# Kernel optimization log

Measured on AMD Instinct MI355X. Metric: run time of the kernel, lower is better.

Reference implementation:

```python
import jax, jax.numpy as jnp
import numpy as np

B, H, L, D = 4, 16, 2048, 128


def setup_inputs() -> dict:
    key = jax.random.key(0)
    kx, kw1, kb1, kw2, kb2 = jax.random.split(key, 5)
    s = 1.0 / np.sqrt(D)
    return {
        "x": jax.random.normal(kx, (B, H, L, D), dtype=jnp.float32),
        "W1": jax.random.uniform(kw1, (D, D), jnp.float32, -s, s),
        "b1": jax.random.uniform(kb1, (D,), jnp.float32, -s, s),
        "W2": jax.random.uniform(kw2, (D, D), jnp.float32, -s, s),
        "b2": jax.random.uniform(kb2, (D,), jnp.float32, -s, s),
    }


def reference(x, W1, b1, W2, b2):
    # proj_1/proj_2: Linear(dim, dim) on the last axis (torch stores W as [out,in])
    q = jnp.einsum('bhld,ed->bhle', x, W1) + b1  # [B,H,L,D]
    k = jnp.einsum('bhld,ed->bhle', x, W2) + b2  # [B,H,L,D]
    # exact-erf GELU on raw QK^T scores, then softmax over j
    adj = jax.nn.gelu(jnp.einsum('bhid,bhjd->bhij', q, k), approximate=False)
    adj = jax.nn.softmax(adj, axis=-1)  # [B,H,L,L]
    # dropout is identity in eval mode
    out = jnp.einsum('bhij,bhjd->bhid', adj, x)  # [B,H,L,D]
    return out.transpose(0, 2, 1, 3).reshape(B, L, H * D)
```

## Files before the change

### kernel.cpp

```cpp
#include <hip/hip_runtime.h>
#include <hip/hip_bf16.h>

#define B_ 4
#define H_ 16
#define L_ 2048
#define D_ 128
#define BH_ 64

typedef __attribute__((ext_vector_type(8))) _Float16 f16x8;
typedef __attribute__((ext_vector_type(4))) float f32x4;
typedef __attribute__((ext_vector_type(16))) float f32x16;
typedef __attribute__((ext_vector_type(2))) unsigned u32x2;

#define L2E 1.44269504088896f

__device__ __forceinline__ float gelu_m(float v, float negm) {
  float x    = v * 0.70710678118f;
  float ax   = __builtin_fabsf(x);
  float t    = __builtin_amdgcn_rcpf(__builtin_fmaf(0.3275911f, ax, 1.0f));
  float poly = t * __builtin_fmaf(t,
                 __builtin_fmaf(t,
                   __builtin_fmaf(t,
                     __builtin_fmaf(t, 1.061405429f, -1.453152027f),
                   1.421413741f),
                 -0.284496736f),
               0.254829592f);
  float nv   = -0.72134752f * v;
  float e    = __builtin_amdgcn_exp2f(nv * v);
  float hva  = __builtin_fabsf(nv);
  float relm = fmaxf(__builtin_fmaf(1.44269504f, v, negm), negm);
  float pe   = poly * e;
  return __builtin_fmaf(hva, -pe, relm);
}

__device__ __forceinline__ void gl2lds16(const void* g, void* l) {
  __builtin_amdgcn_global_load_lds(
      (const __attribute__((address_space(1))) void*)g,
      (__attribute__((address_space(3))) void*)l, 16, 0, 0);
}

__device__ __forceinline__ unsigned pkrtz(float a, float b) {
  auto t = __builtin_amdgcn_cvt_pkrtz(a, b);
  return __builtin_bit_cast(unsigned, t);
}

__global__ __launch_bounds__(256) void wcvt_kernel(
    const float* __restrict__ W1, const float* __restrict__ W2,
    _Float16* __restrict__ Wh1, _Float16* __restrict__ Wh2)
{
  int i = blockIdx.x * 256 + threadIdx.x;
  Wh1[i] = (_Float16)W1[i];
  Wh2[i] = (_Float16)W2[i];
}

__global__ __launch_bounds__(256) void proj_tr_kernel(
    const float* __restrict__ x,
    const _Float16* __restrict__ Wh1, const float* __restrict__ b1,
    const _Float16* __restrict__ Wh2, const float* __restrict__ b2,
    _Float16* __restrict__ Qb, _Float16* __restrict__ Kb,
    _Float16* __restrict__ VT)
{
  const int tid  = threadIdx.x;
  const int wave = tid >> 6;
  const int lane = tid & 63;
  const int lhi  = lane >> 4;
  const int llo  = lane & 15;
  const int r0   = blockIdx.x * 64;
  const int wr0  = r0 + wave * 16;

  f16x8 a[4];
#pragma unroll
  for (int ks = 0; ks < 4; ++ks) {
    const float* p = x + (size_t)(wr0 + llo) * D_ + lhi * 8 + ks * 32;
    f16x8 t;
#pragma unroll
    for (int e = 0; e < 8; ++e) t[e] = (_Float16)p[e];
    a[ks] = t;
  }

  f32x4 accq[8], acck[8];
#pragma unroll
  for (int n = 0; n < 8; ++n) {
    accq[n] = (f32x4){0.f, 0.f, 0.f, 0.f};
    acck[n] = (f32x4){0.f, 0.f, 0.f, 0.f};
  }

#pragma unroll
  for (int n = 0; n < 8; ++n) {
    const int e = n * 16 + llo;
#pragma unroll
    for (int ks = 0; ks < 4; ++ks) {
      f16x8 w1f = *(const f16x8*)(Wh1 + (size_t)e * D_ + lhi * 8 + ks * 32);
      f16x8 w2f = *(const f16x8*)(Wh2 + (size_t)e * D_ + lhi * 8 + ks * 32);
      accq[n] = __builtin_amdgcn_mfma_f32_16x16x32_f16(a[ks], w1f, accq[n], 0, 0, 0);
      acck[n] = __builtin_amdgcn_mfma_f32_16x16x32_f16(a[ks], w2f, acck[n], 0, 0, 0);
    }
  }

#pragma unroll
  for (int n = 0; n < 8; ++n) {
    const int e = n * 16 + llo;
    const float bias1 = b1[e];
    const float bias2 = b2[e];
#pragma unroll
    for (int r = 0; r < 4; ++r) {
      const size_t row = (size_t)wr0 + lhi * 4 + r;
      Qb[row * D_ + e] = (_Float16)(accq[n][r] + bias1);
      Kb[row * D_ + e] = (_Float16)(acck[n][r] + bias2);
    }
  }

  const int bh = r0 / L_;
  const int l0 = r0 % L_;
  const int d  = tid & 127;
  const int rh = tid >> 7;
  _Float16* dst = VT + (size_t)bh * D_ * L_ + (size_t)d * L_ + l0 + rh * 32;
#pragma unroll
  for (int j = 0; j < 4; ++j) {
    f16x8 t;
#pragma unroll
    for (int e = 0; e < 8; ++e)
      t[e] = (_Float16)x[(size_t)(r0 + rh * 32 + j * 8 + e) * D_ + d];
    *(f16x8*)(dst + j * 8) = t;
  }
}

__global__ __launch_bounds__(512) void attn_kernel(
    const _Float16* __restrict__ Qb, const _Float16* __restrict__ Kb,
    const _Float16* __restrict__ VT, float* __restrict__ out)
{
  __shared__ _Float16 Ks[2][64 * 128];
  __shared__ _Float16 Vs[2][128 * 64];

  const int tid  = threadIdx.x;
  const int wave = tid >> 6;
  const int lane = tid & 63;
  const int l5   = lane & 31;
  const int hi   = lane >> 5;

  const int bid = blockIdx.x;
  const int blk = (bid & 7) * 64 + (bid >> 3);
  const int bh  = blk >> 3;
  const int q0  = (blk & 7) * 256;
  const int b   = bh >> 4;
  const int h   = bh & 15;
  const int wq0 = q0 + wave * 32;

  const char* KheadB = (const char*)(Kb + (size_t)bh * L_ * D_);
  const char* VheadB = (const char*)(VT + (size_t)bh * D_ * L_);

  int klds[2], ksrc[2], vlds[2], vsrc[2];
#pragma unroll
  for (int c = 0; c < 2; ++c) {
    const int wc = wave * 2 + c;
    klds[c] = wc * 1024;
    {
      const int l  = wc * 4 + (lane >> 4);
      const int c0 = (lane & 15) * 8;
      ksrc[c] = l * 256 + 2 * (c0 ^ ((l & 7) << 3));
    }
    vlds[c] = wc * 1024;
    {
      const int d  = wc * 8 + (lane >> 3);
      const int c0 = (lane & 7) * 8;
      vsrc[c] = d * 4096 + 2 * (c0 ^ ((d & 7) << 3));
    }
  }
  const int kvswz = (l5 & 7) << 3;

  f16x8 qf[8];
#pragma unroll
  for (int s = 0; s < 8; ++s)
    qf[s] = *(const f16x8*)(Qb + ((size_t)bh * L_ + wq0 + l5) * D_ + s * 16 + hi * 8);

  f32x16 accO[4];
#pragma unroll
  for (int n = 0; n < 4; ++n)
#pragma unroll
    for (int r = 0; r < 16; ++r) accO[n][r] = 0.f;
  float negm = 64.f;
  float l = 0.f;

#pragma unroll
  for (int c = 0; c < 2; ++c) {
    gl2lds16(KheadB + ksrc[c], (char*)&Ks[0][0] + klds[c]);
    gl2lds16(VheadB + vsrc[c], (char*)&Vs[0][0] + vlds[c]);
  }
  __syncthreads();

  int cur = 0;
  for (int t = 0; t < L_ / 64; ++t) {
    if (t + 1 < L_ / 64) {
      const char* kt_ = KheadB + (size_t)(t + 1) * 64 * 256;
      const char* vt_ = VheadB + (size_t)(t + 1) * 128;
#pragma unroll
      for (int c = 0; c < 2; ++c) {
        gl2lds16(kt_ + ksrc[c], (char*)&Ks[cur ^ 1][0] + klds[c]);
        gl2lds16(vt_ + vsrc[c], (char*)&Vs[cur ^ 1][0] + vlds[c]);
      }
    }
    const _Float16* Kcur = &Ks[cur][0];
    const _Float16* Vcur = &Vs[cur][0];

#pragma unroll
    for (int kb = 0; kb < 2; ++kb) {
      f32x16 sT;
#pragma unroll
      for (int r = 0; r < 16; ++r) sT[r] = 0.f;
      __builtin_amdgcn_s_setprio(1);
#pragma unroll
      for (int s = 0; s < 8; ++s) {
        f16x8 kf = *(const f16x8*)(Kcur + (kb * 32 + l5) * 128 +
                                   ((s * 16 + hi * 8) ^ kvswz));
        sT = __builtin_amdgcn_mfma_f32_32x32x16_f16(kf, qf[s], sT, 0, 0, 0);
      }
      __builtin_amdgcn_s_setprio(0);

      float gm[16];
#pragma unroll
      for (int r = 0; r < 16; ++r) gm[r] = gelu_m(sT[r], negm);

      float tm = fmaxf(fmaxf(gm[0], gm[1]), gm[2]);
      tm = fmaxf(fmaxf(tm, gm[3]),  gm[4]);
      tm = fmaxf(fmaxf(tm, gm[5]),  gm[6]);
      tm = fmaxf(fmaxf(tm, gm[7]),  gm[8]);
      tm = fmaxf(fmaxf(tm, gm[9]),  gm[10]);
      tm = fmaxf(fmaxf(tm, gm[11]), gm[12]);
      tm = fmaxf(fmaxf(tm, gm[13]), gm[14]);
      tm = fmaxf(tm, gm[15]);
      tm = fmaxf(tm, __shfl_xor(tm, 32));

      float p[16];
      float ts;
      if (__all(tm <= 11.5415603f)) {
#pragma unroll
        for (int r = 0; r < 16; ++r) p[r] = __builtin_amdgcn_exp2f(gm[r]);
        float a0 = p[0]+p[1],   a1 = p[2]+p[3],   a2 = p[4]+p[5],   a3 = p[6]+p[7];
        float a4 = p[8]+p[9],   a5 = p[10]+p[11], a6 = p[12]+p[13], a7 = p[14]+p[15];
        ts = ((a0+a1)+(a2+a3)) + ((a4+a5)+(a6+a7));
        ts += __shfl_xor(ts, 32);
        l += ts;
      } else {
        float dm = fmaxf(tm, 0.f);
        negm -= dm;
        float sc = __builtin_amdgcn_exp2f(-dm);
#pragma unroll
        for (int r = 0; r < 16; ++r) p[r] = __builtin_amdgcn_exp2f(gm[r] - dm);
        float a0 = p[0]+p[1],   a1 = p[2]+p[3],   a2 = p[4]+p[5],   a3 = p[6]+p[7];
        float a4 = p[8]+p[9],   a5 = p[10]+p[11], a6 = p[12]+p[13], a7 = p[14]+p[15];
        ts = ((a0+a1)+(a2+a3)) + ((a4+a5)+(a6+a7));
        ts += __shfl_xor(ts, 32);
        l = __builtin_fmaf(l, sc, ts);
        float scr[16];
#pragma unroll
        for (int r = 0; r < 16; ++r)
          scr[r] = __shfl(sc, (r & 3) + 8 * (r >> 2) + 4 * hi);
#pragma unroll
        for (int n = 0; n < 4; ++n)
#pragma unroll
          for (int r = 0; r < 16; ++r) accO[n][r] *= scr[r];
      }

      unsigned pk01 = pkrtz(p[0], p[1]),   pk23 = pkrtz(p[2], p[3]);
      unsigned pk45 = pkrtz(p[4], p[5]),   pk67 = pkrtz(p[6], p[7]);
      unsigned pk89 = pkrtz(p[8], p[9]),   pkAB = pkrtz(p[10], p[11]);
      unsigned pkCD = pkrtz(p[12], p[13]), pkEF = pkrtz(p[14], p[15]);
      u32x2 r0 = __builtin_amdgcn_permlane32_swap(pk01, pk45, false, false);
      u32x2 r1 = __builtin_amdgcn_permlane32_swap(pk23, pk67, false, false);
      u32x2 r2 = __builtin_amdgcn_permlane32_swap(pk89, pkCD, false, false);
      u32x2 r3 = __builtin_amdgcn_permlane32_swap(pkAB, pkEF, false, false);
      union { unsigned u[4]; f16x8 v; } A0c, A1c;
      A0c.u[0] = r0[0]; A0c.u[1] = r1[0]; A0c.u[2] = r0[1]; A0c.u[3] = r1[1];
      A1c.u[0] = r2[0]; A1c.u[1] = r3[0]; A1c.u[2] = r2[1]; A1c.u[3] = r3[1];

      __builtin_amdgcn_s_setprio(1);
#pragma unroll
      for (int n = 0; n < 4; ++n) {
        f16x8 vf0 = *(const f16x8*)(Vcur + (n * 32 + l5) * 64 +
                                    ((kb * 32 + hi * 8) ^ kvswz));
        accO[n] = __builtin_amdgcn_mfma_f32_32x32x16_f16(A0c.v, vf0, accO[n], 0, 0, 0);
        f16x8 vf1 = *(const f16x8*)(Vcur + (n * 32 + l5) * 64 +
                                    ((kb * 32 + 16 + hi * 8) ^ kvswz));
        accO[n] = __builtin_amdgcn_mfma_f32_32x32x16_f16(A1c.v, vf1, accO[n], 0, 0, 0);
      }
      __builtin_amdgcn_s_setprio(0);
    }

    __syncthreads();
    cur ^= 1;
  }

  float linv = __builtin_amdgcn_rcpf(l);
  float lb[16];
#pragma unroll
  for (int r = 0; r < 16; ++r)
    lb[r] = __shfl(linv, (r & 3) + 8 * (r >> 2) + 4 * hi);
#pragma unroll
  for (int n = 0; n < 4; ++n)
#pragma unroll
    for (int r = 0; r < 16; ++r) {
      const int i = wq0 + (r & 3) + 8 * (r >> 2) + 4 * hi;
      out[((size_t)(b * L_ + i) * H_ + h) * D_ + n * 32 + l5] = accO[n][r] * lb[r];
    }
}

extern "C" void kernel_launch(void* const* d_in, const int* in_sizes, int n_in,
                              void* d_out, int out_size, void* d_ws, size_t ws_size,
                              hipStream_t stream) {
  const float* x  = (const float*)d_in[0];
  const float* W1 = (const float*)d_in[1];
  const float* b1 = (const float*)d_in[2];
  const float* W2 = (const float*)d_in[3];
  const float* b2 = (const float*)d_in[4];
  float* out = (float*)d_out;

  const size_t N = (size_t)BH_ * L_ * D_;
  _Float16* Qb = (_Float16*)d_ws;
  _Float16* Kb = Qb + N;
  _Float16* VT = Kb + N;

  _Float16* Wh1 = (_Float16*)d_out;
  _Float16* Wh2 = Wh1 + D_ * D_;

  wcvt_kernel<<<64, 256, 0, stream>>>(W1, W2, Wh1, Wh2);
  proj_tr_kernel<<<(BH_ * L_) / 64, 256, 0, stream>>>(x, Wh1, b1, Wh2, b2, Qb, Kb, VT);
  attn_kernel<<<BH_ * (L_ / 256), 512, 0, stream>>>(Qb, Kb, VT, out);
}
```

Before: 383.4 us.

## Halve attention tile sizes and use a cheaper rational erf approximation for GELU

```diff
diff --git a/kernel.cpp b/kernel.cpp
--- a/kernel.cpp
+++ b/kernel.cpp
@@ -15,22 +15,20 @@
 #define L2E 1.44269504088896f
 
 __device__ __forceinline__ float gelu_m(float v, float negm) {
-  float x    = v * 0.70710678118f;
-  float ax   = __builtin_fabsf(x);
-  float t    = __builtin_amdgcn_rcpf(__builtin_fmaf(0.3275911f, ax, 1.0f));
-  float poly = t * __builtin_fmaf(t,
-                 __builtin_fmaf(t,
-                   __builtin_fmaf(t,
-                     __builtin_fmaf(t, 1.061405429f, -1.453152027f),
-                   1.421413741f),
-                 -0.284496736f),
-               0.254829592f);
-  float nv   = -0.72134752f * v;
-  float e    = __builtin_amdgcn_exp2f(nv * v);
-  float hva  = __builtin_fabsf(nv);
-  float relm = fmaxf(__builtin_fmaf(1.44269504f, v, negm), negm);
-  float pe   = poly * e;
-  return __builtin_fmaf(hva, -pe, relm);
+  float x  = __builtin_fabsf(v) * 0.70710678118f;
+  float s  = __builtin_fmaf(x,
+               __builtin_fmaf(x,
+                 __builtin_fmaf(x,
+                   __builtin_fmaf(x, 0.078108f, 0.000972f),
+                 0.230389f),
+               0.278393f),
+             1.0f);
+  float s2 = s * s;
+  float s4 = s2 * s2;
+  float erfa = 1.0f - __builtin_amdgcn_rcpf(s4);
+  float erfv = copysignf(erfa, v);
+  float hv   = 0.72134752f * v;
+  return __builtin_fmaf(hv, erfv, hv + negm);
 }
 
 __device__ __forceinline__ void gl2lds16(const void* g, void* l) {
@@ -125,11 +123,11 @@
   }
 }
 
-__global__ __launch_bounds__(512) void attn_kernel(
+__global__ __launch_bounds__(256) void attn_kernel(
     const _Float16* __restrict__ Qb, const _Float16* __restrict__ Kb,
     const _Float16* __restrict__ VT, float* __restrict__ out)
 {
-  __shared__ _Float16 Ks[2][64 * 128];
+  __shared__ _Float16 Ks[2][32 * 128];
   __shared__ _Float16 Vs[2][128 * 64];
 
   const int tid  = threadIdx.x;
@@ -139,9 +137,9 @@
   const int hi   = lane >> 5;
 
   const int bid = blockIdx.x;
-  const int blk = (bid & 7) * 64 + (bid >> 3);
-  const int bh  = blk >> 3;
-  const int q0  = (blk & 7) * 256;
+  const int blk = (bid & 7) * 128 + (bid >> 3);
+  const int bh  = blk >> 4;
+  const int q0  = (blk & 15) * 128;
   const int b   = bh >> 4;
   const int h   = bh & 15;
   const int wq0 = q0 + wave * 32;
@@ -149,22 +147,21 @@
   const char* KheadB = (const char*)(Kb + (size_t)bh * L_ * D_);
   const char* VheadB = (const char*)(VT + (size_t)bh * D_ * L_);
 
-  int klds[2], ksrc[2], vlds[2], vsrc[2];
+  int kdst[2], ksrc[2];
 #pragma unroll
   for (int c = 0; c < 2; ++c) {
-    const int wc = wave * 2 + c;
-    klds[c] = wc * 1024;
-    {
-      const int l  = wc * 4 + (lane >> 4);
-      const int c0 = (lane & 15) * 8;
-      ksrc[c] = l * 256 + 2 * (c0 ^ ((l & 7) << 3));
-    }
-    vlds[c] = wc * 1024;
-    {
-      const int d  = wc * 8 + (lane >> 3);
-      const int c0 = (lane & 7) * 8;
-      vsrc[c] = d * 4096 + 2 * (c0 ^ ((d & 7) << 3));
-    }
+    kdst[c] = c * 4096 + wave * 1024;
+    const int r  = c * 16 + (tid >> 4);
+    const int h0 = (tid & 15) * 8;
+    ksrc[c] = r * 256 + 2 * (h0 ^ ((r & 7) << 3));
+  }
+  int vdst[4], vsrc[4];
+#pragma unroll
+  for (int c = 0; c < 4; ++c) {
+    vdst[c] = c * 4096 + wave * 1024;
+    const int d  = c * 32 + (tid >> 3);
+    const int h0 = (tid & 7) * 8;
+    vsrc[c] = d * 4096 + 2 * (h0 ^ ((d & 7) << 3));
   }
   const int kvswz = (l5 & 7) << 3;
 
@@ -182,112 +179,113 @@
   float l = 0.f;
 
 #pragma unroll
-  for (int c = 0; c < 2; ++c) {
-    gl2lds16(KheadB + ksrc[c], (char*)&Ks[0][0] + klds[c]);
-    gl2lds16(VheadB + vsrc[c], (char*)&Vs[0][0] + vlds[c]);
-  }
+  for (int c = 0; c < 2; ++c)
+    gl2lds16(KheadB + ksrc[c], (char*)&Ks[0][0] + kdst[c]);
+#pragma unroll
+  for (int c = 0; c < 4; ++c)
+    gl2lds16(VheadB + vsrc[c], (char*)&Vs[0][0] + vdst[c]);
   __syncthreads();
 
-  int cur = 0;
-  for (int t = 0; t < L_ / 64; ++t) {
-    if (t + 1 < L_ / 64) {
-      const char* kt_ = KheadB + (size_t)(t + 1) * 64 * 256;
-      const char* vt_ = VheadB + (size_t)(t + 1) * 128;
-#pragma unroll
-      for (int c = 0; c < 2; ++c) {
-        gl2lds16(kt_ + ksrc[c], (char*)&Ks[cur ^ 1][0] + klds[c]);
-        gl2lds16(vt_ + vsrc[c], (char*)&Vs[cur ^ 1][0] + vlds[c]);
-      }
-    }
-    const _Float16* Kcur = &Ks[cur][0];
-    const _Float16* Vcur = &Vs[cur][0];
-
-#pragma unroll
-    for (int kb = 0; kb < 2; ++kb) {
-      f32x16 sT;
-#pragma unroll
-      for (int r = 0; r < 16; ++r) sT[r] = 0.f;
-      __builtin_amdgcn_s_setprio(1);
-#pragma unroll
-      for (int s = 0; s < 8; ++s) {
-        f16x8 kf = *(const f16x8*)(Kcur + (kb * 32 + l5) * 128 +
-                                   ((s * 16 + hi * 8) ^ kvswz));
-        sT = __builtin_amdgcn_mfma_f32_32x32x16_f16(kf, qf[s], sT, 0, 0, 0);
-      }
-      __builtin_amdgcn_s_setprio(0);
-
-      float gm[16];
-#pragma unroll
-      for (int r = 0; r < 16; ++r) gm[r] = gelu_m(sT[r], negm);
-
-      float tm = fmaxf(fmaxf(gm[0], gm[1]), gm[2]);
-      tm = fmaxf(fmaxf(tm, gm[3]),  gm[4]);
-      tm = fmaxf(fmaxf(tm, gm[5]),  gm[6]);
-      tm = fmaxf(fmaxf(tm, gm[7]),  gm[8]);
-      tm = fmaxf(fmaxf(tm, gm[9]),  gm[10]);
-      tm = fmaxf(fmaxf(tm, gm[11]), gm[12]);
-      tm = fmaxf(fmaxf(tm, gm[13]), gm[14]);
-      tm = fmaxf(tm, gm[15]);
-      tm = fmaxf(tm, __shfl_xor(tm, 32));
-
-      float p[16];
-      float ts;
-      if (__all(tm <= 11.5415603f)) {
-#pragma unroll
-        for (int r = 0; r < 16; ++r) p[r] = __builtin_amdgcn_exp2f(gm[r]);
-        float a0 = p[0]+p[1],   a1 = p[2]+p[3],   a2 = p[4]+p[5],   a3 = p[6]+p[7];
-        float a4 = p[8]+p[9],   a5 = p[10]+p[11], a6 = p[12]+p[13], a7 = p[14]+p[15];
-        ts = ((a0+a1)+(a2+a3)) + ((a4+a5)+(a6+a7));
-        ts += __shfl_xor(ts, 32);
-        l += ts;
-      } else {
-        float dm = fmaxf(tm, 0.f);
-        negm -= dm;
-        float sc = __builtin_amdgcn_exp2f(-dm);
-#pragma unroll
-        for (int r = 0; r < 16; ++r) p[r] = __builtin_amdgcn_exp2f(gm[r] - dm);
-        float a0 = p[0]+p[1],   a1 = p[2]+p[3],   a2 = p[4]+p[5],   a3 = p[6]+p[7];
-        float a4 = p[8]+p[9],   a5 = p[10]+p[11], a6 = p[12]+p[13], a7 = p[14]+p[15];
-        ts = ((a0+a1)+(a2+a3)) + ((a4+a5)+(a6+a7));
-        ts += __shfl_xor(ts, 32);
-        l = __builtin_fmaf(l, sc, ts);
-        float scr[16];
-#pragma unroll
-        for (int r = 0; r < 16; ++r)
-          scr[r] = __shfl(sc, (r & 3) + 8 * (r >> 2) + 4 * hi);
-#pragma unroll
-        for (int n = 0; n < 4; ++n)
-#pragma unroll
-          for (int r = 0; r < 16; ++r) accO[n][r] *= scr[r];
-      }
-
-      unsigned pk01 = pkrtz(p[0], p[1]),   pk23 = pkrtz(p[2], p[3]);
-      unsigned pk45 = pkrtz(p[4], p[5]),   pk67 = pkrtz(p[6], p[7]);
-      unsigned pk89 = pkrtz(p[8], p[9]),   pkAB = pkrtz(p[10], p[11]);
-      unsigned pkCD = pkrtz(p[12], p[13]), pkEF = pkrtz(p[14], p[15]);
-      u32x2 r0 = __builtin_amdgcn_permlane32_swap(pk01, pk45, false, false);
-      u32x2 r1 = __builtin_amdgcn_permlane32_swap(pk23, pk67, false, false);
-      u32x2 r2 = __builtin_amdgcn_permlane32_swap(pk89, pkCD, false, false);
-      u32x2 r3 = __builtin_amdgcn_permlane32_swap(pkAB, pkEF, false, false);
-      union { unsigned u[4]; f16x8 v; } A0c, A1c;
-      A0c.u[0] = r0[0]; A0c.u[1] = r1[0]; A0c.u[2] = r0[1]; A0c.u[3] = r1[1];
-      A1c.u[0] = r2[0]; A1c.u[1] = r3[0]; A1c.u[2] = r2[1]; A1c.u[3] = r3[1];
-
-      __builtin_amdgcn_s_setprio(1);
-#pragma unroll
-      for (int n = 0; n < 4; ++n) {
-        f16x8 vf0 = *(const f16x8*)(Vcur + (n * 32 + l5) * 64 +
-                                    ((kb * 32 + hi * 8) ^ kvswz));
-        accO[n] = __builtin_amdgcn_mfma_f32_32x32x16_f16(A0c.v, vf0, accO[n], 0, 0, 0);
-        f16x8 vf1 = *(const f16x8*)(Vcur + (n * 32 + l5) * 64 +
-                                    ((kb * 32 + 16 + hi * 8) ^ kvswz));
-        accO[n] = __builtin_amdgcn_mfma_f32_32x32x16_f16(A1c.v, vf1, accO[n], 0, 0, 0);
-      }
-      __builtin_amdgcn_s_setprio(0);
-    }
+  for (int t = 0; t < L_ / 32; ++t) {
+    const int kcur = t & 1;
+    const int vcur = (t >> 1) & 1;
+    if (t + 1 < L_ / 32) {
+      const char* kt_ = KheadB + (size_t)(t + 1) * 8192;
+#pragma unroll
+      for (int c = 0; c < 2; ++c)
+        gl2lds16(kt_ + ksrc[c], (char*)&Ks[kcur ^ 1][0] + kdst[c]);
+    }
+    if ((t & 1) == 0 && (t >> 1) + 1 < L_ / 64) {
+      const char* vt_ = VheadB + (size_t)((t >> 1) + 1) * 128;
+#pragma unroll
+      for (int c = 0; c < 4; ++c)
+        gl2lds16(vt_ + vsrc[c], (char*)&Vs[vcur ^ 1][0] + vdst[c]);
+    }
+    const _Float16* Kcur = &Ks[kcur][0];
+    const _Float16* Vcur = &Vs[vcur][0];
+    const int vkbase = (t & 1) * 32;
+
+    f32x16 sT;
+#pragma unroll
+    for (int r = 0; r < 16; ++r) sT[r] = 0.f;
+    __builtin_amdgcn_s_setprio(1);
+#pragma unroll
+    for (int s = 0; s < 8; ++s) {
+      f16x8 kf = *(const f16x8*)(Kcur + l5 * 128 + ((s * 16 + hi * 8) ^ kvswz));
+      sT = __builtin_amdgcn_mfma_f32_32x32x16_f16(kf, qf[s], sT, 0, 0, 0);
+    }
+    __builtin_amdgcn_s_setprio(0);
+
+    float gm[16];
+#pragma unroll
+    for (int r = 0; r < 16; ++r) gm[r] = gelu_m(sT[r], negm);
+
+    float tm = fmaxf(fmaxf(gm[0], gm[1]), gm[2]);
+    tm = fmaxf(fmaxf(tm, gm[3]),  gm[4]);
+    tm = fmaxf(fmaxf(tm, gm[5]),  gm[6]);
+    tm = fmaxf(fmaxf(tm, gm[7]),  gm[8]);
+    tm = fmaxf(fmaxf(tm, gm[9]),  gm[10]);
+    tm = fmaxf(fmaxf(tm, gm[11]), gm[12]);
+    tm = fmaxf(fmaxf(tm, gm[13]), gm[14]);
+    tm = fmaxf(tm, gm[15]);
+    tm = fmaxf(tm, __shfl_xor(tm, 32));
+
+    float p[16];
+    float ts;
+    if (__all(tm <= 11.5415603f)) {
+#pragma unroll
+      for (int r = 0; r < 16; ++r) p[r] = __builtin_amdgcn_exp2f(gm[r]);
+      float a0 = p[0]+p[1],   a1 = p[2]+p[3],   a2 = p[4]+p[5],   a3 = p[6]+p[7];
+      float a4 = p[8]+p[9],   a5 = p[10]+p[11], a6 = p[12]+p[13], a7 = p[14]+p[15];
+      ts = ((a0+a1)+(a2+a3)) + ((a4+a5)+(a6+a7));
+      ts += __shfl_xor(ts, 32);
+      l += ts;
+    } else {
+      float dm = fmaxf(tm, 0.f);
+      negm -= dm;
+      float sc = __builtin_amdgcn_exp2f(-dm);
+#pragma unroll
+      for (int r = 0; r < 16; ++r) p[r] = __builtin_amdgcn_exp2f(gm[r] - dm);
+      float a0 = p[0]+p[1],   a1 = p[2]+p[3],   a2 = p[4]+p[5],   a3 = p[6]+p[7];
+      float a4 = p[8]+p[9],   a5 = p[10]+p[11], a6 = p[12]+p[13], a7 = p[14]+p[15];
+      ts = ((a0+a1)+(a2+a3)) + ((a4+a5)+(a6+a7));
+      ts += __shfl_xor(ts, 32);
+      l = __builtin_fmaf(l, sc, ts);
+      float scr[16];
+#pragma unroll
+      for (int r = 0; r < 16; ++r)
+        scr[r] = __shfl(sc, (r & 3) + 8 * (r >> 2) + 4 * hi);
+#pragma unroll
+      for (int n = 0; n < 4; ++n)
+#pragma unroll
+        for (int r = 0; r < 16; ++r) accO[n][r] *= scr[r];
+    }
+
+    unsigned pk01 = pkrtz(p[0], p[1]),   pk23 = pkrtz(p[2], p[3]);
+    unsigned pk45 = pkrtz(p[4], p[5]),   pk67 = pkrtz(p[6], p[7]);
+    unsigned pk89 = pkrtz(p[8], p[9]),   pkAB = pkrtz(p[10], p[11]);
+    unsigned pkCD = pkrtz(p[12], p[13]), pkEF = pkrtz(p[14], p[15]);
+    u32x2 r0 = __builtin_amdgcn_permlane32_swap(pk01, pk45, false, false);
+    u32x2 r1 = __builtin_amdgcn_permlane32_swap(pk23, pk67, false, false);
+    u32x2 r2 = __builtin_amdgcn_permlane32_swap(pk89, pkCD, false, false);
+    u32x2 r3 = __builtin_amdgcn_permlane32_swap(pkAB, pkEF, false, false);
+    union { unsigned u[4]; f16x8 v; } A0c, A1c;
+    A0c.u[0] = r0[0]; A0c.u[1] = r1[0]; A0c.u[2] = r0[1]; A0c.u[3] = r1[1];
+    A1c.u[0] = r2[0]; A1c.u[1] = r3[0]; A1c.u[2] = r2[1]; A1c.u[3] = r3[1];
+
+    __builtin_amdgcn_s_setprio(1);
+#pragma unroll
+    for (int n = 0; n < 4; ++n) {
+      f16x8 vf0 = *(const f16x8*)(Vcur + (n * 32 + l5) * 64 +
+                                  ((vkbase + hi * 8) ^ kvswz));
+      accO[n] = __builtin_amdgcn_mfma_f32_32x32x16_f16(A0c.v, vf0, accO[n], 0, 0, 0);
+      f16x8 vf1 = *(const f16x8*)(Vcur + (n * 32 + l5) * 64 +
+                                  ((vkbase + 16 + hi * 8) ^ kvswz));
+      accO[n] = __builtin_amdgcn_mfma_f32_32x32x16_f16(A1c.v, vf1, accO[n], 0, 0, 0);
+    }
+    __builtin_amdgcn_s_setprio(0);
 
     __syncthreads();
-    cur ^= 1;
   }
 
   float linv = __builtin_amdgcn_rcpf(l);
@@ -324,5 +322,5 @@
 
   wcvt_kernel<<<64, 256, 0, stream>>>(W1, W2, Wh1, Wh2);
   proj_tr_kernel<<<(BH_ * L_) / 64, 256, 0, stream>>>(x, Wh1, b1, Wh2, b2, Qb, Kb, VT);
-  attn_kernel<<<BH_ * (L_ / 256), 512, 0, stream>>>(Qb, Kb, VT, out);
-}
+  attn_kernel<<<BH_ * (L_ / 128), 256, 0, stream>>>(Qb, Kb, VT, out);
+}
```

Result: slower. 535.3 us (+39.6%).

## Use cheaper erf approximation in GELU and split QK^T MFMA chain into two accumulators

Applied to the files above, without the earlier changes.

```diff
diff --git a/kernel.cpp b/kernel.cpp
--- a/kernel.cpp
+++ b/kernel.cpp
@@ -15,22 +15,20 @@
 #define L2E 1.44269504088896f
 
 __device__ __forceinline__ float gelu_m(float v, float negm) {
-  float x    = v * 0.70710678118f;
-  float ax   = __builtin_fabsf(x);
-  float t    = __builtin_amdgcn_rcpf(__builtin_fmaf(0.3275911f, ax, 1.0f));
-  float poly = t * __builtin_fmaf(t,
-                 __builtin_fmaf(t,
-                   __builtin_fmaf(t,
-                     __builtin_fmaf(t, 1.061405429f, -1.453152027f),
-                   1.421413741f),
-                 -0.284496736f),
-               0.254829592f);
-  float nv   = -0.72134752f * v;
-  float e    = __builtin_amdgcn_exp2f(nv * v);
-  float hva  = __builtin_fabsf(nv);
-  float relm = fmaxf(__builtin_fmaf(1.44269504f, v, negm), negm);
-  float pe   = poly * e;
-  return __builtin_fmaf(hva, -pe, relm);
+  float x  = __builtin_fabsf(v) * 0.70710678118f;
+  float s  = __builtin_fmaf(x,
+               __builtin_fmaf(x,
+                 __builtin_fmaf(x,
+                   __builtin_fmaf(x, 0.078108f, 0.000972f),
+                 0.230389f),
+               0.278393f),
+             1.0f);
+  float s2 = s * s;
+  float s4 = s2 * s2;
+  float erfa = 1.0f - __builtin_amdgcn_rcpf(s4);
+  float erfv = copysignf(erfa, v);
+  float hv   = 0.72134752f * v;
+  return __builtin_fmaf(hv, erfv, hv + negm);
 }
 
 __device__ __forceinline__ void gl2lds16(const void* g, void* l) {
@@ -204,21 +202,24 @@
 
 #pragma unroll
     for (int kb = 0; kb < 2; ++kb) {
-      f32x16 sT;
-#pragma unroll
-      for (int r = 0; r < 16; ++r) sT[r] = 0.f;
+      f32x16 sTa, sTb;
+#pragma unroll
+      for (int r = 0; r < 16; ++r) { sTa[r] = 0.f; sTb[r] = 0.f; }
       __builtin_amdgcn_s_setprio(1);
 #pragma unroll
-      for (int s = 0; s < 8; ++s) {
-        f16x8 kf = *(const f16x8*)(Kcur + (kb * 32 + l5) * 128 +
-                                   ((s * 16 + hi * 8) ^ kvswz));
-        sT = __builtin_amdgcn_mfma_f32_32x32x16_f16(kf, qf[s], sT, 0, 0, 0);
+      for (int s = 0; s < 4; ++s) {
+        f16x8 kfa = *(const f16x8*)(Kcur + (kb * 32 + l5) * 128 +
+                                    ((s * 16 + hi * 8) ^ kvswz));
+        sTa = __builtin_amdgcn_mfma_f32_32x32x16_f16(kfa, qf[s], sTa, 0, 0, 0);
+        f16x8 kfb = *(const f16x8*)(Kcur + (kb * 32 + l5) * 128 +
+                                    (((s + 4) * 16 + hi * 8) ^ kvswz));
+        sTb = __builtin_amdgcn_mfma_f32_32x32x16_f16(kfb, qf[s + 4], sTb, 0, 0, 0);
       }
       __builtin_amdgcn_s_setprio(0);
 
       float gm[16];
 #pragma unroll
-      for (int r = 0; r < 16; ++r) gm[r] = gelu_m(sT[r], negm);
+      for (int r = 0; r < 16; ++r) gm[r] = gelu_m(sTa[r] + sTb[r], negm);
 
       float tm = fmaxf(fmaxf(gm[0], gm[1]), gm[2]);
       tm = fmaxf(fmaxf(tm, gm[3]),  gm[4]);
```

Measured after the change: 370.1 us. -3.5%, faster.
